# Kernel optimization log

Measured on AMD Instinct MI355X. Metric: run time of the kernel, lower is better.

## Reference

```python
import jax, jax.numpy as jnp
import numpy as np

H = 128  # rnn_size

def setup_inputs() -> dict:
    key = jax.random.key(0)
    ks = jax.random.split(key, 12)
    B, T, F = 64, 2048, 64
    s = lambda k, shape, fan: jax.random.normal(k, shape, jnp.float32) * (1.0 / np.sqrt(fan))
    return {
        "x":  jax.random.normal(ks[0], (B, T, F), jnp.float32),
        # LSTM params (Keras gate order: i, f, c(g), o)
        "W":  s(ks[1], (F, 4 * H), F),
        "U":  s(ks[2], (H, 4 * H), H),
        "b":  jnp.zeros((4 * H,), jnp.float32),
        # Dense stack
        "W1": s(ks[3], (H, 128), H),   "b1": jnp.zeros((128,), jnp.float32),
        "W2": s(ks[4], (128, 128), 128), "b2": jnp.zeros((128,), jnp.float32),
        "W3": s(ks[5], (128, 32), 128),  "b3": jnp.zeros((32,), jnp.float32),
        "W4": s(ks[6], (32, 1), 32),     "b4": jnp.zeros((1,), jnp.float32),
    }

def _lstm(x, W, U, b):
    # x: [B,T,F] -> outputs h_t for all t: [B,T,H]
    B, T, _ = x.shape
    xp = jnp.einsum('btf,fg->btg', x, W) + b        # precompute input projection [B,T,4H]
    xp = jnp.transpose(xp, (1, 0, 2))               # [T,B,4H] for scan

    def step(carry, xt):
        h, c = carry
        z = xt + h @ U                              # [B,4H]
        i, f, g, o = jnp.split(z, 4, axis=-1)       # Keras gate order i,f,c,o
        i = jax.nn.sigmoid(i)
        f = jax.nn.sigmoid(f)
        g = jnp.tanh(g)
        o = jax.nn.sigmoid(o)
        c = f * c + i * g
        h = o * jnp.tanh(c)
        return (h, c), h

    h0 = jnp.zeros((B, H), x.dtype)
    c0 = jnp.zeros((B, H), x.dtype)
    _, hs = jax.lax.scan(step, (h0, c0), xp)        # hs: [T,B,H]
    return jnp.transpose(hs, (1, 0, 2))             # [B,T,H]

def reference(x, W, U, b, W1, b1, W2, b2, W3, b3, W4, b4):
    h = _lstm(x, W, U, b)                           # [B,T,H]
    h = h @ W1 + b1                                 # d1 (linear)
    h = jax.nn.relu(h @ W2 + b2)                    # d2
    h = jax.nn.relu(h @ W3 + b3)                    # d3
    out = jax.nn.sigmoid(h @ W4 + b4)               # d4 -> [B,T,1]
    return out.reshape(out.shape[0], -1, 1)         # Reshape((-1,1)) is identity here
```

## Files before the change

kernel.cpp:

```cpp
#include <hip/hip_runtime.h>
#include <hip/hip_fp16.h>
#include <cstdint>
#include <cstddef>

typedef _Float16 hh2   __attribute__((ext_vector_type(2)));
typedef _Float16 f16x8 __attribute__((ext_vector_type(8)));
typedef float    f32x4 __attribute__((ext_vector_type(4)));
typedef int      i32x4 __attribute__((ext_vector_type(4)));

__device__ __forceinline__ float fdot2u(unsigned a, unsigned b, float c) {
#if __has_builtin(__builtin_amdgcn_fdot2)
    return __builtin_amdgcn_fdot2(__builtin_bit_cast(hh2, a),
                                  __builtin_bit_cast(hh2, b), c, false);
#else
    float r;
    asm("v_dot2_f32_f16 %0, %1, %2, %3" : "=v"(r) : "v"(a), "v"(b), "v"(c));
    return r;
#endif
}

__device__ __forceinline__ unsigned packh2f(float x, float y) {
    hh2 v; v.x = (_Float16)x; v.y = (_Float16)y;
    return __builtin_bit_cast(unsigned, v);
}

__device__ __forceinline__ float ex2(float x) {
#if __has_builtin(__builtin_amdgcn_exp2f)
    return __builtin_amdgcn_exp2f(x);
#else
    return exp2f(x);
#endif
}
__device__ __forceinline__ float sig2(float x) {
    return __builtin_amdgcn_rcpf(1.f + ex2(x * -1.442695041f));
}
__device__ __forceinline__ float tanh2(float x) {
    return fmaf(2.f, __builtin_amdgcn_rcpf(1.f + ex2(x * -2.885390082f)), -1.f);
}
__device__ __forceinline__ float sigmoidf_fast(float x) {
    return __builtin_amdgcn_rcpf(1.f + __expf(-x));
}
__device__ __forceinline__ float tanhf_fast(float x) {
    float e = __expf(-2.f * fmaxf(x, -30.f));
    return (1.f - e) * __builtin_amdgcn_rcpf(1.f + e);
}

#define BAR_LGKM() asm volatile("s_waitcnt lgkmcnt(0)\n\ts_barrier" ::: "memory")

__global__ __launch_bounds__(512, 2)
void k_xprojT(const float* __restrict__ x, const float* __restrict__ W,
              const float* __restrict__ bias, __half* __restrict__ xpT,
              int B, int T)
{
    __shared__ unsigned short xst[2][16 * 64];

    const int tid = threadIdx.x;
    const int w   = tid >> 6;
    const int l   = tid & 63;
    const int lj  = l & 15;
    const int hi  = l >> 4;
    const int bb  = blockIdx.x >> 2;
    const int q   = blockIdx.x & 3;

    f16x8 Wf[4][2];
    float bc[4];
#pragma unroll
    for (int cg = 0; cg < 4; ++cg) {
        const int col = cg * 128 + w * 16 + lj;
#pragma unroll
        for (int kk = 0; kk < 2; ++kk)
#pragma unroll
            for (int j = 0; j < 8; ++j)
                Wf[cg][kk][j] = (_Float16)W[(size_t)(kk*32 + hi*8 + j) * 512 + col];
        bc[cg] = bias[col];
    }

    const int nch = (T / 4) / 16;
    const size_t rowbase = (size_t)bb * T + (size_t)q * (T / 4);

    const int srow = tid >> 5;
    const int scp  = tid & 31;

    float2 xn = *(const float2*)(x + (rowbase + srow) * 64 + scp * 2);

    for (int ch = 0; ch < nch; ++ch) {
        unsigned pk = packh2f(xn.x, xn.y);
        *(unsigned*)((char*)xst[ch & 1] +
            (((srow * 128 + scp * 4)) ^ ((srow & 7) << 4))) = pk;
        if (ch + 1 < nch)
            xn = *(const float2*)(x + (rowbase + (ch+1)*16 + srow) * 64 + scp * 2);
        BAR_LGKM();

        f16x8 Axf[2];
#pragma unroll
        for (int kk = 0; kk < 2; ++kk)
            Axf[kk] = *(const f16x8*)((char*)xst[ch & 1] +
                ((lj * 128 + kk * 64 + hi * 16) ^ ((lj & 7) << 4)));

        const size_t c8base = (rowbase + (size_t)ch * 16) >> 3;
#pragma unroll
        for (int cg = 0; cg < 4; ++cg) {
            f32x4 C = {bc[cg], bc[cg], bc[cg], bc[cg]};
            C = __builtin_amdgcn_mfma_f32_16x16x32_f16(Axf[0], Wf[cg][0], C, 0, 0, 0);
            C = __builtin_amdgcn_mfma_f32_16x16x32_f16(Axf[1], Wf[cg][1], C, 0, 0, 0);
            const int col = cg * 128 + w * 16 + lj;
            uint2 u;
            u.x = packh2f(C[0], C[1]);
            u.y = packh2f(C[2], C[3]);
            const size_t hidx = ((c8base + (hi >> 1)) * 512 + col) * 8 + (hi & 1) * 4;
            *(uint2*)((unsigned short*)xpT + hidx) = u;
        }
        BAR_LGKM();
    }
}

__global__ __launch_bounds__(512, 2)
void k_lstm8(const float* __restrict__ U, const __half* __restrict__ xpT,
             __half* __restrict__ hs, int T)
{
    __shared__ unsigned char hbuf[2][128];
    __shared__ float exch[512];

    const int tid = threadIdx.x;
    const int w   = tid >> 6;
    const int l   = tid & 63;
    const int lj  = l & 15;
    const int hi  = l >> 4;
    const int bb  = blockIdx.x;

    i32x4 Bq[4][2];
    float um[4];
#pragma unroll
    for (int g = 0; g < 4; ++g) {
        const int col = g * 128 + w * 16 + lj;
        float m = 0.f;
        for (int k2 = 0; k2 < 128; ++k2)
            m = fmaxf(m, fabsf(U[(size_t)k2 * 512 + col]));
        um[g] = m;
        const float s = (m > 0.f) ? 127.f / m : 0.f;
#pragma unroll
        for (int kk = 0; kk < 2; ++kk) {
            int wds[4];
#pragma unroll
            for (int d = 0; d < 4; ++d) {
                unsigned word = 0;
#pragma unroll
                for (int b = 0; b < 4; ++b) {
                    int qv = (int)rintf(
                        U[(size_t)(kk*64 + hi*16 + d*4 + b) * 512 + col] * s);
                    word |= (unsigned)(qv & 255) << (8 * b);
                }
                wds[d] = (int)word;
            }
            Bq[g][kk] = (i32x4){wds[0], wds[1], wds[2], wds[3]};
        }
    }

    const float um_me = (hi & 2) ? ((hi & 1) ? um[3] : um[2])
                                 : ((hi & 1) ? um[1] : um[0]);
    const float dq_me = um_me * (1.f / (127.f * 127.f));
    const float mlt = (hi == 2) ? -2.885390082f : -1.442695041f;
    const float pa  = (hi == 2) ? 2.f : 1.f;
    const float pb  = (hi == 2) ? -1.f : 0.f;

    if (tid < 32) ((unsigned*)hbuf[0])[tid] = 0u;

    const uint4* __restrict__ xb = (const uint4*)xpT;
    const size_t xrow = (size_t)bb * (T / 8) * 512;
    const int col_me = hi * 128 + w * 16 + lj;

    uint4 qA = xb[xrow + 0 * 512 + col_me];
    uint4 qB = xb[xrow + 1 * 512 + col_me];

    __half* __restrict__ hsb = hs + (size_t)bb * T * 128;
    float cst = 0.f;

    float* exw = &exch[w * 64 + lj * 4 + hi];
    const float* exr = &exch[w * 64 + lj * 4];

    i32x4 Cq[4] = {{0,0,0,0},{0,0,0,0},{0,0,0,0},{0,0,0,0}};

    __syncthreads();

    const int nbody = T / 16;
    for (int k = 0; k < nbody; ++k) {
#pragma unroll
        for (int p = 0; p < 16; ++p) {
            if (p == 8)
                qA = xb[xrow + (size_t)(2*k + 2) * 512 + col_me];

            const unsigned char* hrow = hbuf[p & 1];
            i32x4 Aq0 = *(const i32x4*)(hrow + hi * 16);
            i32x4 Aq1 = *(const i32x4*)(hrow + 64 + hi * 16);

            Cq[0][0] = 0; Cq[1][0] = 0; Cq[2][0] = 0; Cq[3][0] = 0;
#pragma unroll
            for (int g = 0; g < 4; ++g) {
                Cq[g] = __builtin_amdgcn_mfma_i32_16x16x64_i8(Aq0, Bq[g][0], Cq[g], 0, 0, 0);
                Cq[g] = __builtin_amdgcn_mfma_i32_16x16x64_i8(Aq1, Bq[g][1], Cq[g], 0, 0, 0);
            }

            int zi = (hi & 2) ? ((hi & 1) ? Cq[3][0] : Cq[2][0])
                              : ((hi & 1) ? Cq[1][0] : Cq[0][0]);

            const uint4 qq = (p < 8) ? qA : qB;
            const int wsel = (p & 7) >> 1;
            unsigned uw = (wsel == 0) ? qq.x : (wsel == 1) ? qq.y
                        : (wsel == 2) ? qq.z : qq.w;
            __half2 hh = __builtin_bit_cast(__half2, uw);
            float xpf = __half2float((p & 1) ? __high2half(hh) : __low2half(hh));

            float zf = fmaf((float)zi, dq_me, xpf);

            float e = ex2(zf * mlt);
            float a = fmaf(pa, __builtin_amdgcn_rcpf(1.f + e), pb);

            *exw = a;
            f32x4 v = *(const f32x4*)exr;

            cst = fmaf(v[1], cst, v[0] * v[2]);
            float h = v[3] * tanh2(cst);

            if (l < 16) {
                hbuf[(p & 1) ^ 1][w * 16 + lj] =
                    (unsigned char)(int)rintf(h * 127.f);
                hsb[(size_t)(k * 16 + p) * 128 + w * 16 + lj] = __float2half(h);
            }

            if (p == 15)
                qB = xb[xrow + (size_t)(2*k + 3) * 512 + col_me];
            BAR_LGKM();
        }
    }
}

__global__ __launch_bounds__(512, 2)
void k_head(const __half* __restrict__ hs,
            const float* __restrict__ W1, const float* __restrict__ b1,
            const float* __restrict__ W2, const float* __restrict__ b2,
            const float* __restrict__ W3, const float* __restrict__ b3,
            const float* __restrict__ W4, const float* __restrict__ b4,
            float* __restrict__ out, int T)
{
    __shared__ unsigned short hstage[16 * 128];
    __shared__ unsigned short d1buf[16 * 128];
    __shared__ unsigned short d2buf[16 * 128];
    __shared__ unsigned short d3buf[16 * 40];

    const int tid = threadIdx.x;
    const int w   = tid >> 6;
    const int l   = tid & 63;
    const int lj  = l & 15;
    const int hi  = l >> 4;
    const int bb  = blockIdx.x >> 5;
    const int ch0 = (blockIdx.x & 31) * 4;

    const int col1 = w * 16 + lj;
    const int col3 = (w & 1) * 16 + lj;

    f16x8 W1f[4], W2f[4], W3f[4];
#pragma unroll
    for (int kk = 0; kk < 4; ++kk)
#pragma unroll
        for (int j = 0; j < 8; ++j) {
            W1f[kk][j] = (_Float16)W1[(size_t)(kk*32 + hi*8 + j) * 128 + col1];
            W2f[kk][j] = (_Float16)W2[(size_t)(kk*32 + hi*8 + j) * 128 + col1];
            W3f[kk][j] = (_Float16)W3[(size_t)(kk*32 + hi*8 + j) * 32 + col3];
        }
    const float b1c = b1[col1];
    const float b2c = b2[col1];
    const float b3c = b3[col3];
    unsigned w4p[16];
#pragma unroll
    for (int k2 = 0; k2 < 16; ++k2)
        w4p[k2] = packh2f(W4[2*k2], W4[2*k2 + 1]);
    const float b4v = b4[0];

    const __half* __restrict__ hsb = hs + (size_t)bb * T * 128;
    const int srow = tid >> 5;
    const int scp  = tid & 31;

    for (int ch = ch0; ch < ch0 + 4; ++ch) {
        const int t0 = ch * 16;
        uint2 hv = *(const uint2*)(hsb + (size_t)(t0 + srow) * 128 + scp * 4);
        *(uint2*)((char*)hstage + ((srow * 256 + scp * 8) ^ ((srow & 7) << 4))) = hv;
        __syncthreads();

        f16x8 A[4];
#pragma unroll
        for (int kk = 0; kk < 4; ++kk)
            A[kk] = *(const f16x8*)((char*)hstage +
                ((lj * 256 + kk * 64 + hi * 16) ^ ((lj & 7) << 4)));
        f32x4 C1 = {b1c, b1c, b1c, b1c};
#pragma unroll
        for (int kk = 0; kk < 4; ++kk)
            C1 = __builtin_amdgcn_mfma_f32_16x16x32_f16(A[kk], W1f[kk], C1, 0, 0, 0);
#pragma unroll
        for (int r = 0; r < 4; ++r) {
            const int row = hi * 4 + r;
            *(unsigned short*)((char*)d1buf + ((row * 256 + col1 * 2) ^ ((row & 7) << 4))) =
                __half_as_ushort(__float2half(C1[r]));
        }
        __syncthreads();

#pragma unroll
        for (int kk = 0; kk < 4; ++kk)
            A[kk] = *(const f16x8*)((char*)d1buf +
                ((lj * 256 + kk * 64 + hi * 16) ^ ((lj & 7) << 4)));
        f32x4 C2 = {b2c, b2c, b2c, b2c};
#pragma unroll
        for (int kk = 0; kk < 4; ++kk)
            C2 = __builtin_amdgcn_mfma_f32_16x16x32_f16(A[kk], W2f[kk], C2, 0, 0, 0);
#pragma unroll
        for (int r = 0; r < 4; ++r) {
            const int row = hi * 4 + r;
            *(unsigned short*)((char*)d2buf + ((row * 256 + col1 * 2) ^ ((row & 7) << 4))) =
                __half_as_ushort(__float2half(fmaxf(C2[r], 0.f)));
        }
        __syncthreads();

#pragma unroll
        for (int kk = 0; kk < 4; ++kk)
            A[kk] = *(const f16x8*)((char*)d2buf +
                ((lj * 256 + kk * 64 + hi * 16) ^ ((lj & 7) << 4)));
        f32x4 C3 = {b3c, b3c, b3c, b3c};
#pragma unroll
        for (int kk = 0; kk < 4; ++kk)
            C3 = __builtin_amdgcn_mfma_f32_16x16x32_f16(A[kk], W3f[kk], C3, 0, 0, 0);
        if (w < 2) {
#pragma unroll
            for (int r = 0; r < 4; ++r) {
                const int row = hi * 4 + r;
                d3buf[row * 40 + col3] =
                    __half_as_ushort(__float2half(fmaxf(C3[r], 0.f)));
            }
        }
        __syncthreads();

        if (w == 0 && l < 16) {
            const unsigned short* dr = &d3buf[l * 40];
            float s0 = b4v, s1 = 0.f;
#pragma unroll
            for (int qq = 0; qq < 4; ++qq) {
                uint4 v = *(const uint4*)(dr + qq * 8);
                s0 = fdot2u(v.x, w4p[qq*4 + 0], s0);
                s1 = fdot2u(v.y, w4p[qq*4 + 1], s1);
                s0 = fdot2u(v.z, w4p[qq*4 + 2], s0);
                s1 = fdot2u(v.w, w4p[qq*4 + 3], s1);
            }
            out[(size_t)bb * T + t0 + l] = sigmoidf_fast(s0 + s1);
        }
        __syncthreads();
    }
}

__global__ __launch_bounds__(512)
void k_lstm_fused(const float* __restrict__ U, const float* __restrict__ x,
                  const float* __restrict__ W, const float* __restrict__ bias,
                  __half* __restrict__ hs, int T)
{
    __shared__ __align__(16) unsigned hbuf[64];
    __shared__ float act[512];
    __shared__ __align__(16) unsigned xrow[32];

    const int g    = threadIdx.x;
    const int bb   = blockIdx.x;
    const int j    = g & 127;
    const int gate = g >> 7;

    unsigned ucol[64];
#pragma unroll
    for (int k2 = 0; k2 < 64; ++k2)
        ucol[k2] = packh2f(U[(2*k2)*512 + g], U[(2*k2+1)*512 + g]);
    unsigned wcol[32];
#pragma unroll
    for (int k2 = 0; k2 < 32; ++k2)
        wcol[k2] = packh2f(W[(2*k2)*512 + g], W[(2*k2+1)*512 + g]);
    const float bg = bias[g];
    const float2* __restrict__ xb2 = (const float2*)(x + (size_t)bb * T * 64);
    if (g < 32) { float2 x0 = xb2[g]; xrow[g] = packh2f(x0.x, x0.y); }
    if (g < 64) hbuf[g] = 0u;
    float c = 0.f;
    __half* __restrict__ hsb = hs + (size_t)bb * T * 128;
    __syncthreads();

    for (int t = 0; t < T; ++t) {
        float2 xn = make_float2(0.f, 0.f);
        if (g < 32 && t + 1 < T) xn = xb2[(size_t)(t + 1) * 32 + g];
        float a0 = bg, a1 = 0.f, a2 = 0.f, a3 = 0.f;
        const uint4* hr = (const uint4*)hbuf;
#pragma unroll
        for (int k8 = 0; k8 < 16; ++k8) {
            uint4 v = hr[k8];
            a0 = fdot2u(v.x, ucol[4*k8+0], a0);
            a1 = fdot2u(v.y, ucol[4*k8+1], a1);
            a2 = fdot2u(v.z, ucol[4*k8+2], a2);
            a3 = fdot2u(v.w, ucol[4*k8+3], a3);
        }
        const uint4* xr = (const uint4*)xrow;
#pragma unroll
        for (int k8 = 0; k8 < 8; ++k8) {
            uint4 v = xr[k8];
            a0 = fdot2u(v.x, wcol[4*k8+0], a0);
            a1 = fdot2u(v.y, wcol[4*k8+1], a1);
            a2 = fdot2u(v.z, wcol[4*k8+2], a2);
            a3 = fdot2u(v.w, wcol[4*k8+3], a3);
        }
        float z = (a0 + a1) + (a2 + a3);
        float a = (gate == 2) ? tanhf_fast(z) : sigmoidf_fast(z);
        act[g] = a;
        __syncthreads();
        float iv = act[j], fv = act[j + 128], gv = act[j + 256], ov = act[j + 384];
        c = fmaf(fv, c, iv * gv);
        float h = ov * tanhf_fast(c);
        if (gate == 0) {
            ((unsigned short*)hbuf)[j] = __half_as_ushort(__float2half(h));
            hsb[(size_t)t * 128 + j] = __float2half(h);
        }
        if (g < 32 && t + 1 < T) xrow[g] = packh2f(xn.x, xn.y);
        __syncthreads();
    }
}

template<bool RELU>
__global__ __launch_bounds__(512)
void k_fc128(const __half* __restrict__ in16, const float* __restrict__ Wg,
             const float* __restrict__ bias, __half* __restrict__ out16, int rows)
{
    __shared__ __align__(16) unsigned rowbuf[4 * 64];
    const int tid = threadIdx.x;
    const int n   = tid & 127;
    const int rs  = tid >> 7;
    unsigned wcol[64];
#pragma unroll
    for (int k2 = 0; k2 < 64; ++k2)
        wcol[k2] = packh2f(Wg[(2*k2)*128 + n], Wg[(2*k2+1)*128 + n]);
    const float bn = bias[n];
    for (int row0 = blockIdx.x * 4; row0 < rows; row0 += gridDim.x * 4) {
        if (tid < 256)
            rowbuf[tid] = ((const unsigned*)(in16 + (size_t)row0 * 128))[tid];
        __syncthreads();
        float a0 = bn, a1 = 0.f, a2 = 0.f, a3 = 0.f;
        const uint4* hr = (const uint4*)(rowbuf + rs * 64);
#pragma unroll
        for (int k8 = 0; k8 < 16; ++k8) {
            uint4 v = hr[k8];
            a0 = fdot2u(v.x, wcol[4*k8+0], a0);
            a1 = fdot2u(v.y, wcol[4*k8+1], a1);
            a2 = fdot2u(v.z, wcol[4*k8+2], a2);
            a3 = fdot2u(v.w, wcol[4*k8+3], a3);
        }
        float a = (a0 + a1) + (a2 + a3);
        if (RELU) a = fmaxf(a, 0.f);
        out16[(size_t)(row0 + rs) * 128 + n] = __float2half(a);
        __syncthreads();
    }
}

__global__ __launch_bounds__(512)
void k_l34(const __half* __restrict__ in16, const float* __restrict__ W3,
           const float* __restrict__ b3, const float* __restrict__ W4,
           const float* __restrict__ b4, float* __restrict__ out, int rows)
{
    __shared__ __align__(16) unsigned rowbuf[16 * 64];
    __shared__ __align__(16) unsigned short d3s[16 * 32];
    const int tid = threadIdx.x;
    const int n   = tid & 31;
    const int rs  = tid >> 5;
    unsigned w3col[64];
#pragma unroll
    for (int k2 = 0; k2 < 64; ++k2)
        w3col[k2] = packh2f(W3[(2*k2)*32 + n], W3[(2*k2+1)*32 + n]);
    unsigned w4p[16];
#pragma unroll
    for (int k2 = 0; k2 < 16; ++k2)
        w4p[k2] = packh2f(W4[2*k2], W4[2*k2+1]);
    const float b3n = b3[n], b4v = b4[0];
    for (int row0 = blockIdx.x * 16; row0 < rows; row0 += gridDim.x * 16) {
        rowbuf[tid]       = ((const unsigned*)(in16 + (size_t)row0 * 128))[tid];
        rowbuf[tid + 512] = ((const unsigned*)(in16 + (size_t)row0 * 128))[tid + 512];
        __syncthreads();
        float a0 = b3n, a1 = 0.f, a2 = 0.f, a3 = 0.f;
        const uint4* hr = (const uint4*)(rowbuf + rs * 64);
#pragma unroll
        for (int k8 = 0; k8 < 16; ++k8) {
            uint4 v = hr[k8];
            a0 = fdot2u(v.x, w3col[4*k8+0], a0);
            a1 = fdot2u(v.y, w3col[4*k8+1], a1);
            a2 = fdot2u(v.z, w3col[4*k8+2], a2);
            a3 = fdot2u(v.w, w3col[4*k8+3], a3);
        }
        float a = fmaxf((a0 + a1) + (a2 + a3), 0.f);
        d3s[rs * 32 + n] = __half_as_ushort(__float2half(a));
        __syncthreads();
        if (tid < 16) {
            const uint4* dp = (const uint4*)(d3s + tid * 32);
            float s0 = b4v, s1 = 0.f;
#pragma unroll
            for (int qq = 0; qq < 4; ++qq) {
                uint4 v = dp[qq];
                s0 = fdot2u(v.x, w4p[4*qq+0], s0);
                s1 = fdot2u(v.y, w4p[4*qq+1], s1);
                s0 = fdot2u(v.z, w4p[4*qq+2], s0);
                s1 = fdot2u(v.w, w4p[4*qq+3], s1);
            }
            out[row0 + tid] = sigmoidf_fast(s0 + s1);
        }
        __syncthreads();
    }
}

extern "C" void kernel_launch(void* const* d_in, const int* in_sizes, int n_in,
                              void* d_out, int out_size, void* d_ws, size_t ws_size,
                              hipStream_t stream)
{
    const float* x  = (const float*)d_in[0];
    const float* W  = (const float*)d_in[1];
    const float* U  = (const float*)d_in[2];
    const float* b  = (const float*)d_in[3];
    const float* W1 = (const float*)d_in[4];
    const float* b1 = (const float*)d_in[5];
    const float* W2 = (const float*)d_in[6];
    const float* b2 = (const float*)d_in[7];
    const float* W3 = (const float*)d_in[8];
    const float* b3 = (const float*)d_in[9];
    const float* W4 = (const float*)d_in[10];
    const float* b4 = (const float*)d_in[11];
    float* out = (float*)d_out;

    const int T    = 2048;
    const int rows = in_sizes[0] / 64;
    const int B    = rows / T;

    char* ws = (char*)d_ws;
    const size_t xp_bytes = (size_t)rows * 512 * sizeof(__half);
    const size_t hs_bytes = (size_t)rows * 128 * sizeof(__half);

    if (ws_size >= xp_bytes + hs_bytes) {
        __half* xpT  = (__half*)ws;
        __half* hs16 = (__half*)(ws + xp_bytes);
        k_xprojT<<<B * 4, 512, 0, stream>>>(x, W, b, xpT, B, T);
        k_lstm8<<<B, 512, 0, stream>>>(U, xpT, hs16, T);
        k_head<<<B * 32, 512, 0, stream>>>(hs16, W1, b1, W2, b2, W3, b3,
                                           W4, b4, out, T);
    } else {
        __half* hs16 = (__half*)ws;
        __half* d1   = (__half*)(ws + hs_bytes);
        __half* d2   = (__half*)ws;
        k_lstm_fused<<<B, 512, 0, stream>>>(U, x, W, b, hs16, T);
        k_fc128<false><<<1024, 512, 0, stream>>>(hs16, W1, b1, d1, rows);
        k_fc128<true ><<<1024, 512, 0, stream>>>(d1,  W2, b2, d2, rows);
        k_l34<<<1024, 512, 0, stream>>>(d2, W3, b3, W4, b4, out, rows);
    }
}
```

Before: 792.7 us.

## Pack two batch rows per 1024-thread block and exchange gates via lane permutes

The LSTM recurrence kernel now runs two batch sequences per block of 16 waves, halving the block count. The LDS round-trip used to gather the four gate activations is replaced by a ds_swizzle and a permlane32_swap, with the gate-to-row mapping reordered so that partner lanes hold matching gates. The aim is to shorten the serial per-timestep critical path by removing LDS store/load latency. The cost is that the barrier now spans twice as many waves, and it only applies when B is even.

```diff
diff --git a/kernel.cpp b/kernel.cpp
--- a/kernel.cpp
+++ b/kernel.cpp
@@ -7,6 +7,7 @@
 typedef _Float16 f16x8 __attribute__((ext_vector_type(8)));
 typedef float    f32x4 __attribute__((ext_vector_type(4)));
 typedef int      i32x4 __attribute__((ext_vector_type(4)));
+typedef int      v2i   __attribute__((ext_vector_type(2)));
 
 __device__ __forceinline__ float fdot2u(unsigned a, unsigned b, float c) {
 #if __has_builtin(__builtin_amdgcn_fdot2)
@@ -114,25 +115,28 @@
     }
 }
 
-__global__ __launch_bounds__(512, 2)
-void k_lstm8(const float* __restrict__ U, const __half* __restrict__ xpT,
+__global__ __launch_bounds__(1024, 4)
+void k_lstm9(const float* __restrict__ U, const __half* __restrict__ xpT,
              __half* __restrict__ hs, int T)
 {
-    __shared__ unsigned char hbuf[2][128];
-    __shared__ float exch[512];
+    __shared__ unsigned char hbuf[2][2][128];
 
     const int tid = threadIdx.x;
     const int w   = tid >> 6;
     const int l   = tid & 63;
     const int lj  = l & 15;
     const int hi  = l >> 4;
-    const int bb  = blockIdx.x;
+    const int bat = (w ^ (w >> 2)) & 1;
+    const int cg  = w >> 1;
+    const int bb  = blockIdx.x * 2 + bat;
+
+    const int g_me = (hi == 1) ? 2 : (hi == 2) ? 1 : hi;
 
     i32x4 Bq[4][2];
     float um[4];
 #pragma unroll
     for (int g = 0; g < 4; ++g) {
-        const int col = g * 128 + w * 16 + lj;
+        const int col = g * 128 + cg * 16 + lj;
         float m = 0.f;
         for (int k2 = 0; k2 < 128; ++k2)
             m = fmaxf(m, fabsf(U[(size_t)k2 * 512 + col]));
@@ -156,27 +160,24 @@
         }
     }
 
-    const float um_me = (hi & 2) ? ((hi & 1) ? um[3] : um[2])
-                                 : ((hi & 1) ? um[1] : um[0]);
+    const float um_me = (hi == 1) ? um[2] : (hi == 2) ? um[1]
+                      : (hi == 3) ? um[3] : um[0];
     const float dq_me = um_me * (1.f / (127.f * 127.f));
-    const float mlt = (hi == 2) ? -2.885390082f : -1.442695041f;
-    const float pa  = (hi == 2) ? 2.f : 1.f;
-    const float pb  = (hi == 2) ? -1.f : 0.f;
-
-    if (tid < 32) ((unsigned*)hbuf[0])[tid] = 0u;
+    const float mlt = (hi == 1) ? -2.885390082f : -1.442695041f;
+    const float pa  = (hi == 1) ? 2.f : 1.f;
+    const float pb  = (hi == 1) ? -1.f : 0.f;
+
+    if (tid < 128) ((unsigned*)hbuf)[tid] = 0u;
 
     const uint4* __restrict__ xb = (const uint4*)xpT;
     const size_t xrow = (size_t)bb * (T / 8) * 512;
-    const int col_me = hi * 128 + w * 16 + lj;
+    const int col_me = g_me * 128 + cg * 16 + lj;
 
     uint4 qA = xb[xrow + 0 * 512 + col_me];
     uint4 qB = xb[xrow + 1 * 512 + col_me];
 
     __half* __restrict__ hsb = hs + (size_t)bb * T * 128;
     float cst = 0.f;
-
-    float* exw = &exch[w * 64 + lj * 4 + hi];
-    const float* exr = &exch[w * 64 + lj * 4];
 
     i32x4 Cq[4] = {{0,0,0,0},{0,0,0,0},{0,0,0,0},{0,0,0,0}};
 
@@ -189,7 +190,7 @@
             if (p == 8)
                 qA = xb[xrow + (size_t)(2*k + 2) * 512 + col_me];
 
-            const unsigned char* hrow = hbuf[p & 1];
+            const unsigned char* hrow = &hbuf[bat][p & 1][0];
             i32x4 Aq0 = *(const i32x4*)(hrow + hi * 16);
             i32x4 Aq1 = *(const i32x4*)(hrow + 64 + hi * 16);
 
@@ -200,8 +201,9 @@
                 Cq[g] = __builtin_amdgcn_mfma_i32_16x16x64_i8(Aq1, Bq[g][1], Cq[g], 0, 0, 0);
             }
 
-            int zi = (hi & 2) ? ((hi & 1) ? Cq[3][0] : Cq[2][0])
-                              : ((hi & 1) ? Cq[1][0] : Cq[0][0]);
+            int a01 = (hi & 1) ? Cq[2][0] : Cq[0][0];
+            int a23 = (hi & 1) ? Cq[3][0] : Cq[1][0];
+            int zi  = (hi & 2) ? a23 : a01;
 
             const uint4 qq = (p < 8) ? qA : qB;
             const int wsel = (p & 7) >> 1;
@@ -215,16 +217,32 @@
             float e = ex2(zf * mlt);
             float a = fmaf(pa, __builtin_amdgcn_rcpf(1.f + e), pb);
 
-            *exw = a;
-            f32x4 v = *(const f32x4*)exr;
-
-            cst = fmaf(v[1], cst, v[0] * v[2]);
-            float h = v[3] * tanh2(cst);
-
-            if (l < 16) {
-                hbuf[(p & 1) ^ 1][w * 16 + lj] =
+            float s1 = __builtin_bit_cast(float,
+                __builtin_amdgcn_ds_swizzle(__builtin_bit_cast(int, a), 0x401F));
+
+            float pv = a * s1;
+            float fv = (hi == 2) ? a : s1;
+            float ov = (hi == 2) ? s1 : a;
+
+#if __has_builtin(__builtin_amdgcn_permlane32_swap)
+            v2i r = __builtin_amdgcn_permlane32_swap(
+                __builtin_bit_cast(int, pv), __builtin_bit_cast(int, pv),
+                false, false);
+            float pc = __builtin_bit_cast(float, r[0]);
+#else
+            __shared__ float pex[16][16];
+            if (hi == 0) pex[w][lj] = pv;
+            asm volatile("s_waitcnt lgkmcnt(0)" ::: "memory");
+            float pc = pex[w][lj];
+#endif
+
+            cst = fmaf(fv, cst, pc);
+            float h = ov * tanh2(cst);
+
+            if (hi == 2) {
+                hbuf[bat][(p & 1) ^ 1][cg * 16 + lj] =
                     (unsigned char)(int)rintf(h * 127.f);
-                hsb[(size_t)(k * 16 + p) * 128 + w * 16 + lj] = __float2half(h);
+                hsb[(size_t)(k * 16 + p) * 128 + cg * 16 + lj] = __float2half(h);
             }
 
             if (p == 15)
@@ -536,11 +554,11 @@
     const size_t xp_bytes = (size_t)rows * 512 * sizeof(__half);
     const size_t hs_bytes = (size_t)rows * 128 * sizeof(__half);
 
-    if (ws_size >= xp_bytes + hs_bytes) {
+    if (ws_size >= xp_bytes + hs_bytes && (B & 1) == 0) {
         __half* xpT  = (__half*)ws;
         __half* hs16 = (__half*)(ws + xp_bytes);
         k_xprojT<<<B * 4, 512, 0, stream>>>(x, W, b, xpT, B, T);
-        k_lstm8<<<B, 512, 0, stream>>>(U, xpT, hs16, T);
+        k_lstm9<<<B / 2, 1024, 0, stream>>>(U, xpT, hs16, T);
         k_head<<<B * 32, 512, 0, stream>>>(hs16, W1, b1, W2, b2, W3, b3,
                                            W4, b4, out, T);
     } else {
```

Result: slower. 1.093 ms (+37.9%).
